# Performance work log

Measured on AMD Instinct MI355X. Metric: run time of the kernel, lower is better.

The kernel has to match this reference:

```python
import jax, jax.numpy as jnp
import numpy as np

TEMPERATURE = 8.0  # sqrt(d_k=64)
MASK_FILL = -1e10


def setup_inputs() -> dict:
    key = jax.random.key(0)
    kq, kk, kv, km = jax.random.split(key, 4)
    b, lq, lk, dk, dv = 32, 2048, 2048, 64, 64
    q = jax.random.normal(kq, (b, lq, dk), dtype=jnp.float32)
    k = jax.random.normal(kk, (b, lk, dk), dtype=jnp.float32)
    v = jax.random.normal(kv, (b, lk, dv), dtype=jnp.float32)
    mask = jax.random.randint(km, (b, lq, lk), 0, 2).astype(jnp.bool_)
    return {"q": q, "k": k, "v": v, "mask": mask}


def reference(q, k, v, mask):
    # attn = q @ k^T / temperature, masked_fill, softmax over keys (dim=2)
    attn = jnp.einsum("bqd,bkd->bqk", q, k) / TEMPERATURE
    attn = jnp.where(mask, MASK_FILL, attn)
    attn = jax.nn.softmax(attn, axis=2)
    # dropout p=0.0 (eval/deterministic reference) -> identity
    output = jnp.einsum("bqk,bkv->bqv", attn, v)
    return (output, attn)
```

## Files before the change

kernel.cpp:

```cpp
#include <hip/hip_runtime.h>
#include <cstdint>
#include <cstddef>

#define B_   32
#define LQ   2048
#define LK   2048
#define DK   64
#define DV   64
#define TQ   16
#define LDP  2056

typedef short bf16x8 __attribute__((ext_vector_type(8)));
typedef float f32x4  __attribute__((ext_vector_type(4)));

#define KSCALE 0.1803368801111204f

__device__ __forceinline__ short f2bf(float f) {
  unsigned u = __builtin_bit_cast(unsigned, f);
  u += 0x7fffu + ((u >> 16) & 1u);
  return (short)(u >> 16);
}
__device__ __forceinline__ float bflo(unsigned u) { return __builtin_bit_cast(float, u << 16); }
__device__ __forceinline__ float bfhi(unsigned u) { return __builtin_bit_cast(float, u & 0xffff0000u); }

__device__ __forceinline__ bf16x8 pack8(float4 a, float4 b) {
  bf16x8 r;
  r[0]=f2bf(a.x); r[1]=f2bf(a.y); r[2]=f2bf(a.z); r[3]=f2bf(a.w);
  r[4]=f2bf(b.x); r[5]=f2bf(b.y); r[6]=f2bf(b.z); r[7]=f2bf(b.w);
  return r;
}

__global__ __launch_bounds__(512, 4) void sdpa_kernel(
    const float* __restrict__ q, const float* __restrict__ k,
    const float* __restrict__ v, const int* __restrict__ mask,
    float* __restrict__ out, float* __restrict__ attn) {
  __shared__ short P[TQ][LDP];
  __shared__ float rowsum[TQ];
  __shared__ float rinv[TQ];

  const int tid  = threadIdx.x;
  const int wave = tid >> 6;
  const int lane = tid & 63;
  const int quad = lane >> 4;
  const int l15  = lane & 15;
  const int b     = blockIdx.y;
  const int qbase = blockIdx.x * TQ;

  if (tid < TQ) rowsum[tid] = 0.0f;
  __syncthreads();

  const float* qr = q + ((size_t)b * LQ + qbase + l15) * DK + quad * 8;
  bf16x8 qa0 = pack8(*(const float4*)(qr),      *(const float4*)(qr + 4));
  bf16x8 qa1 = pack8(*(const float4*)(qr + 32), *(const float4*)(qr + 36));

  const float* kbase = k + (size_t)b * LK * DK + (size_t)l15 * DK + quad * 8;
  const int*   mbase = mask + (size_t)b * LQ * LK + (size_t)(qbase + quad * 4) * LK + l15;
  const f32x4 z4 = {0.f, 0.f, 0.f, 0.f};

  float4 kp0, kp1, kp2, kp3;
  int mp[4];
  int nt = wave;
  {
    const float* kr = kbase + (size_t)nt * (16 * DK);
    kp0 = *(const float4*)(kr);      kp1 = *(const float4*)(kr + 4);
    kp2 = *(const float4*)(kr + 32); kp3 = *(const float4*)(kr + 36);
    const int* mr = mbase + nt * 16;
    #pragma unroll
    for (int r = 0; r < 4; ++r)
      mp[r] = __builtin_nontemporal_load(mr + (size_t)r * LK);
  }
  float sum0[4] = {0,0,0,0};
  #pragma unroll 1
  for (int i = 0; i < 16; ++i) {
    float4 kc0 = kp0, kc1 = kp1, kc2 = kp2, kc3 = kp3;
    int mc[4];
    #pragma unroll
    for (int r = 0; r < 4; ++r) mc[r] = mp[r];
    const int ntc = nt;
    nt += 8;
    if (i != 15) {
      const float* kr = kbase + (size_t)nt * (16 * DK);
      kp0 = *(const float4*)(kr);      kp1 = *(const float4*)(kr + 4);
      kp2 = *(const float4*)(kr + 32); kp3 = *(const float4*)(kr + 36);
      const int* mr = mbase + nt * 16;
      #pragma unroll
      for (int r = 0; r < 4; ++r)
        mp[r] = __builtin_nontemporal_load(mr + (size_t)r * LK);
    }
    bf16x8 kb0 = pack8(kc0, kc1);
    bf16x8 kb1 = pack8(kc2, kc3);
    f32x4 acc0 = __builtin_amdgcn_mfma_f32_16x16x32_bf16(qa0, kb0, z4, 0, 0, 0);
    acc0       = __builtin_amdgcn_mfma_f32_16x16x32_bf16(qa1, kb1, acc0, 0, 0, 0);
    const int col = ntc * 16 + l15;
    #pragma unroll
    for (int r = 0; r < 4; ++r) {
      float p0 = mc[r] ? 0.0f : __builtin_amdgcn_exp2f(acc0[r] * KSCALE);
      P[quad * 4 + r][col] = f2bf(p0);
      sum0[r] += p0;
    }
  }
  #pragma unroll
  for (int r = 0; r < 4; ++r) {
    float s0 = sum0[r];
    #pragma unroll
    for (int off = 1; off < 16; off <<= 1) {
      s0 += __shfl_xor(s0, off);
    }
    if (l15 == 0) {
      atomicAdd(&rowsum[quad * 4 + r], s0);
    }
  }
  __syncthreads();
  if (tid < TQ) rinv[tid] = 1.0f / rowsum[tid];
  __syncthreads();

  if (wave < 4) {
    const float* vbase = v + (size_t)b * LK * DV + wave * 16 + l15;
    f32x4 o0 = z4;
    float fv[8];
    #pragma unroll
    for (int j = 0; j < 8; ++j) fv[j] = vbase[(size_t)(quad * 8 + j) * DV];
    #pragma unroll 1
    for (int kt = 0; kt < 64; ++kt) {
      float fc[8];
      #pragma unroll
      for (int j = 0; j < 8; ++j) fc[j] = fv[j];
      if (kt != 63) {
        #pragma unroll
        for (int j = 0; j < 8; ++j)
          fv[j] = vbase[(size_t)((kt + 1) * 32 + quad * 8 + j) * DV];
      }
      bf16x8 bv;
      #pragma unroll
      for (int j = 0; j < 8; ++j) bv[j] = f2bf(fc[j]);
      bf16x8 a0 = *(const bf16x8*)&P[l15][kt * 32 + quad * 8];
      o0 = __builtin_amdgcn_mfma_f32_16x16x32_bf16(a0, bv, o0, 0, 0, 0);
    }
    #pragma unroll
    for (int r = 0; r < 4; ++r) {
      const int row0 = quad * 4 + r;
      out[((size_t)b * LQ + qbase + row0) * DV + wave * 16 + l15] = o0[r] * rinv[row0];
    }
  } else {
    const int ww = wave - 4;
    float* abase = attn + ((size_t)b * LQ + qbase) * (size_t)LK;
    #pragma unroll 1
    for (int j = 0; j < 4; ++j) {
      const int row = ww * 4 + j;
      const float ri = rinv[row];
      float* dst = abase + (size_t)row * LK;
      #pragma unroll
      for (int it = 0; it < 8; ++it) {
        const int c = it * 256 + lane * 4;
        uint2 u = *(const uint2*)&P[row][c];
        f32x4 val;
        val[0] = bflo(u.x) * ri;
        val[1] = bfhi(u.x) * ri;
        val[2] = bflo(u.y) * ri;
        val[3] = bfhi(u.y) * ri;
        __builtin_nontemporal_store(val, (f32x4*)(dst + c));
      }
    }
  }
}

extern "C" void kernel_launch(void* const* d_in, const int* in_sizes, int n_in,
                              void* d_out, int out_size, void* d_ws, size_t ws_size,
                              hipStream_t stream) {
  (void)in_sizes; (void)n_in; (void)out_size; (void)d_ws; (void)ws_size;
  const float* q    = (const float*)d_in[0];
  const float* k    = (const float*)d_in[1];
  const float* v    = (const float*)d_in[2];
  const int*   mask = (const int*)d_in[3];
  float* out  = (float*)d_out;
  float* attn = out + (size_t)B_ * LQ * DV;
  dim3 grid(LQ / TQ, B_);
  sdpa_kernel<<<grid, 512, 0, stream>>>(q, k, v, mask, out, attn);
}
```

Baseline: 1.251 ms.

## Apply mask in a separate coalesced row pass and double-buffer V loads

The QK loop no longer reads the mask with strided scalar loads. Instead, after the exp values are stored to shared memory, each wave reads two full mask rows with 16-byte nontemporal vector loads. It zeroes the masked bf16 entries in place and computes row sums with a wave-wide shuffle reduction, which replaces the shared-memory atomics. The PV loop is unrolled by two with separate prefetch buffers so more V loads are in flight. The cost is an extra barrier and an extra read-modify-write pass over the P tile in LDS. Row sums are now taken from the bf16-rounded values rather than the fp32 ones.

```diff
diff --git a/kernel.cpp b/kernel.cpp
--- a/kernel.cpp
+++ b/kernel.cpp
@@ -12,6 +12,7 @@
 
 typedef short bf16x8 __attribute__((ext_vector_type(8)));
 typedef float f32x4  __attribute__((ext_vector_type(4)));
+typedef int   i32x4  __attribute__((ext_vector_type(4)));
 
 #define KSCALE 0.1803368801111204f
 
@@ -46,46 +47,29 @@
   const int b     = blockIdx.y;
   const int qbase = blockIdx.x * TQ;
 
-  if (tid < TQ) rowsum[tid] = 0.0f;
-  __syncthreads();
-
   const float* qr = q + ((size_t)b * LQ + qbase + l15) * DK + quad * 8;
   bf16x8 qa0 = pack8(*(const float4*)(qr),      *(const float4*)(qr + 4));
   bf16x8 qa1 = pack8(*(const float4*)(qr + 32), *(const float4*)(qr + 36));
 
   const float* kbase = k + (size_t)b * LK * DK + (size_t)l15 * DK + quad * 8;
-  const int*   mbase = mask + (size_t)b * LQ * LK + (size_t)(qbase + quad * 4) * LK + l15;
   const f32x4 z4 = {0.f, 0.f, 0.f, 0.f};
 
   float4 kp0, kp1, kp2, kp3;
-  int mp[4];
   int nt = wave;
   {
     const float* kr = kbase + (size_t)nt * (16 * DK);
     kp0 = *(const float4*)(kr);      kp1 = *(const float4*)(kr + 4);
     kp2 = *(const float4*)(kr + 32); kp3 = *(const float4*)(kr + 36);
-    const int* mr = mbase + nt * 16;
-    #pragma unroll
-    for (int r = 0; r < 4; ++r)
-      mp[r] = __builtin_nontemporal_load(mr + (size_t)r * LK);
   }
-  float sum0[4] = {0,0,0,0};
   #pragma unroll 1
   for (int i = 0; i < 16; ++i) {
     float4 kc0 = kp0, kc1 = kp1, kc2 = kp2, kc3 = kp3;
-    int mc[4];
-    #pragma unroll
-    for (int r = 0; r < 4; ++r) mc[r] = mp[r];
     const int ntc = nt;
     nt += 8;
     if (i != 15) {
       const float* kr = kbase + (size_t)nt * (16 * DK);
       kp0 = *(const float4*)(kr);      kp1 = *(const float4*)(kr + 4);
       kp2 = *(const float4*)(kr + 32); kp3 = *(const float4*)(kr + 36);
-      const int* mr = mbase + nt * 16;
-      #pragma unroll
-      for (int r = 0; r < 4; ++r)
-        mp[r] = __builtin_nontemporal_load(mr + (size_t)r * LK);
     }
     bf16x8 kb0 = pack8(kc0, kc1);
     bf16x8 kb1 = pack8(kc2, kc3);
@@ -94,21 +78,35 @@
     const int col = ntc * 16 + l15;
     #pragma unroll
     for (int r = 0; r < 4; ++r) {
-      float p0 = mc[r] ? 0.0f : __builtin_amdgcn_exp2f(acc0[r] * KSCALE);
-      P[quad * 4 + r][col] = f2bf(p0);
-      sum0[r] += p0;
+      P[quad * 4 + r][col] = f2bf(__builtin_amdgcn_exp2f(acc0[r] * KSCALE));
     }
   }
+  __syncthreads();
+
   #pragma unroll
-  for (int r = 0; r < 4; ++r) {
-    float s0 = sum0[r];
+  for (int j = 0; j < 2; ++j) {
+    const int row = wave * 2 + j;
+    const int* mrow = mask + ((size_t)b * LQ + qbase + row) * LK + lane * 4;
+    i32x4 mv[8];
     #pragma unroll
-    for (int off = 1; off < 16; off <<= 1) {
-      s0 += __shfl_xor(s0, off);
+    for (int c = 0; c < 8; ++c)
+      mv[c] = __builtin_nontemporal_load((const i32x4*)(mrow + c * 256));
+    float rs = 0.0f;
+    #pragma unroll
+    for (int c = 0; c < 8; ++c) {
+      uint2 u = *(const uint2*)&P[row][c * 256 + lane * 4];
+      unsigned x0 = mv[c][0] ? 0u : (u.x & 0x0000ffffu);
+      unsigned x1 = mv[c][1] ? 0u : (u.x & 0xffff0000u);
+      unsigned y0 = mv[c][2] ? 0u : (u.y & 0x0000ffffu);
+      unsigned y1 = mv[c][3] ? 0u : (u.y & 0xffff0000u);
+      u.x = x0 | x1;
+      u.y = y0 | y1;
+      *(uint2*)&P[row][c * 256 + lane * 4] = u;
+      rs += bflo(u.x) + bfhi(u.x) + bflo(u.y) + bfhi(u.y);
     }
-    if (l15 == 0) {
-      atomicAdd(&rowsum[quad * 4 + r], s0);
-    }
+    #pragma unroll
+    for (int off = 1; off < 64; off <<= 1) rs += __shfl_xor(rs, off);
+    if (lane == 0) rowsum[row] = rs;
   }
   __syncthreads();
   if (tid < TQ) rinv[tid] = 1.0f / rowsum[tid];
@@ -117,24 +115,40 @@
   if (wave < 4) {
     const float* vbase = v + (size_t)b * LK * DV + wave * 16 + l15;
     f32x4 o0 = z4;
-    float fv[8];
+    float fva[8], fvb[8];
     #pragma unroll
-    for (int j = 0; j < 8; ++j) fv[j] = vbase[(size_t)(quad * 8 + j) * DV];
+    for (int j = 0; j < 8; ++j) {
+      fva[j] = vbase[(size_t)(quad * 8 + j) * DV];
+      fvb[j] = vbase[(size_t)(32 + quad * 8 + j) * DV];
+    }
     #pragma unroll 1
-    for (int kt = 0; kt < 64; ++kt) {
+    for (int kt = 0; kt < 64; kt += 2) {
       float fc[8];
       #pragma unroll
-      for (int j = 0; j < 8; ++j) fc[j] = fv[j];
-      if (kt != 63) {
+      for (int j = 0; j < 8; ++j) fc[j] = fva[j];
+      if (kt != 62) {
         #pragma unroll
         for (int j = 0; j < 8; ++j)
-          fv[j] = vbase[(size_t)((kt + 1) * 32 + quad * 8 + j) * DV];
+          fva[j] = vbase[(size_t)((kt + 2) * 32 + quad * 8 + j) * DV];
       }
-      bf16x8 bv;
+      bf16x8 bv0;
       #pragma unroll
-      for (int j = 0; j < 8; ++j) bv[j] = f2bf(fc[j]);
+      for (int j = 0; j < 8; ++j) bv0[j] = f2bf(fc[j]);
       bf16x8 a0 = *(const bf16x8*)&P[l15][kt * 32 + quad * 8];
-      o0 = __builtin_amdgcn_mfma_f32_16x16x32_bf16(a0, bv, o0, 0, 0, 0);
+      o0 = __builtin_amdgcn_mfma_f32_16x16x32_bf16(a0, bv0, o0, 0, 0, 0);
+
+      #pragma unroll
+      for (int j = 0; j < 8; ++j) fc[j] = fvb[j];
+      if (kt != 62) {
+        #pragma unroll
+        for (int j = 0; j < 8; ++j)
+          fvb[j] = vbase[(size_t)((kt + 3) * 32 + quad * 8 + j) * DV];
+      }
+      bf16x8 bv1;
+      #pragma unroll
+      for (int j = 0; j < 8; ++j) bv1[j] = f2bf(fc[j]);
+      bf16x8 a1 = *(const bf16x8*)&P[l15][(kt + 1) * 32 + quad * 8];
+      o0 = __builtin_amdgcn_mfma_f32_16x16x32_bf16(a1, bv1, o0, 0, 0, 0);
     }
     #pragma unroll
     for (int r = 0; r < 4; ++r) {
```

After: 1.268 ms. Within noise of the previous version (+1.3%).
